# Kernel tuning notes

Measured on AMD Instinct MI355X. Metric: run time of the kernel, lower is better.

Reference implementation:

```python
import jax, jax.numpy as jnp
import numpy as np

HEAD_DIM = 128
NUM_BUCKETS = 32
MAX_DISTANCE = 128


def _rel_pos_bucket(seq_len):
    # T5 causal relative-position bucketing (lucidrains flash-pytorch version)
    pos = jnp.arange(seq_len)
    rel = pos[None, :] - pos[:, None]          # k_pos - q_pos
    n = jnp.maximum(-rel, 0)                   # causal: only past distances
    max_exact = NUM_BUCKETS // 2
    is_small = n < max_exact
    n_safe = jnp.maximum(n, 1).astype(jnp.float32)
    val_large = max_exact + (
        jnp.log(n_safe / max_exact) / np.log(MAX_DISTANCE / max_exact)
        * (NUM_BUCKETS - max_exact)
    ).astype(jnp.int32)
    val_large = jnp.minimum(val_large, NUM_BUCKETS - 1)
    return jnp.where(is_small, n, val_large)   # (S, S) int32


def setup_inputs() -> dict:
    key = jax.random.key(0)
    ks = jax.random.split(key, 10)
    B, S, D, I = 4, 2048, 768, 1536
    s = 0.02
    return {
        "x": jax.random.normal(ks[0], (B, S, D), jnp.float32),
        "v_W": jax.random.normal(ks[1], (D, I), jnp.float32) * s,
        "v_b": jnp.zeros((I,), jnp.float32),
        "g_W": jax.random.normal(ks[2], (D, I), jnp.float32) * s,
        "g_b": jnp.zeros((I,), jnp.float32),
        "in_W": jax.random.normal(ks[3], (D, HEAD_DIM), jnp.float32) * s,
        "in_b": jnp.zeros((HEAD_DIM,), jnp.float32),
        "q_gamma": jax.random.normal(ks[4], (HEAD_DIM,), jnp.float32) * s,
        "q_beta": jnp.zeros((HEAD_DIM,), jnp.float32),
        "k_gamma": jax.random.normal(ks[5], (HEAD_DIM,), jnp.float32) * s,
        "k_beta": jnp.zeros((HEAD_DIM,), jnp.float32),
        "out_W": jax.random.normal(ks[6], (I, D), jnp.float32) * s,
        "out_b": jnp.zeros((D,), jnp.float32),
        "rel_emb": jax.random.normal(ks[7], (NUM_BUCKETS, 1), jnp.float32) * s,
    }


def reference(x, v_W, v_b, g_W, g_b, in_W, in_b,
              q_gamma, q_beta, k_gamma, k_beta, out_W, out_b, rel_emb):
    silu = jax.nn.silu
    S = x.shape[1]
    v = silu(x @ v_W + v_b)                    # (B, S, I)
    gate = silu(x @ g_W + g_b)                 # (B, S, I)
    base = silu(x @ in_W + in_b)               # (B, S, 128)
    q = base * q_gamma + q_beta
    k = base * k_gamma + k_beta
    # scores scaled by sqrt(v dim) per torch code (v.size(-1) = inner_dim)
    attn = jnp.einsum('bns,bms->bnm', q, k) / jnp.sqrt(jnp.float32(v.shape[-1]))
    bias = rel_emb[_rel_pos_bucket(S), 0] * np.sqrt(HEAD_DIM)  # (S, S)
    attn = attn + bias
    causal = jnp.triu(jnp.ones((S, S), bool), 1)
    attn = jnp.where(causal, 0.0, attn)        # masked_fill to 0 before relu^2
    attn = jnp.square(jax.nn.relu(attn))       # ReLU^2 attention (no softmax)
    o = jnp.einsum('bnm,bme->bne', attn, v) * gate
    return o @ out_W + out_b                   # (B, S, D)
```

## Files before the change

### kernel.cpp

```cpp
#include <hip/hip_runtime.h>


typedef short short8 __attribute__((ext_vector_type(8)));
typedef float f32x4 __attribute__((ext_vector_type(4)));
typedef unsigned short us4 __attribute__((ext_vector_type(4)));
typedef float fl4 __attribute__((ext_vector_type(4)));

__device__ __forceinline__ unsigned short f2bf(float f) {
  unsigned u = __builtin_bit_cast(unsigned, f);
  u += 0x7FFFu + ((u >> 16) & 1u);
  return (unsigned short)(u >> 16);
}
__device__ __forceinline__ float bf2f(unsigned short b) {
  return __builtin_bit_cast(float, ((unsigned)b) << 16);
}
__device__ __forceinline__ float silu_f(float x) { return x / (1.0f + __expf(-x)); }

__device__ __forceinline__ void gl_lds16(const void* gp, void* lp) {
  __builtin_amdgcn_global_load_lds((const __attribute__((address_space(1))) void*)gp,
                                   (__attribute__((address_space(3))) void*)lp, 16, 0, 0);
}

template <int CALLS>
__device__ __forceinline__ void stage_sw(const unsigned short* __restrict__ g,
                                         int row_stride, int r0, int ko,
                                         unsigned short* lds, int w, int l) {
#pragma unroll
  for (int c = 0; c < CALLS; ++c) {
    int e = ((w * CALLS + c) << 9) + l * 8;
    int row = e >> 6;
    int gcol = ((((e >> 3) & 7) ^ (row & 7)) << 3);
    gl_lds16(g + (size_t)(r0 + row) * row_stride + (ko + gcol), lds + e);
  }
}
__device__ __forceinline__ void stage_sw128(const unsigned short* __restrict__ g, int r0,
                                            unsigned short* lds, int w, int l) {
#pragma unroll
  for (int c = 0; c < 8; ++c) {
    int e = ((w * 8 + c) << 9) + l * 8;
    int row = e >> 7;
    int gcol = ((((e >> 3) & 15) ^ (row & 7)) << 3);
    gl_lds16(g + (size_t)(r0 + row) * 128 + gcol, lds + e);
  }
}

__device__ __forceinline__ void mfma_sw(const unsigned short* As, const unsigned short* Bs,
                                        f32x4 acc[4][4], int wm, int wn, int quad, int lc) {
  const int x7 = lc & 7;
#pragma unroll
  for (int kk = 0; kk < 2; ++kk) {
    short8 af[4], bfr[4];
#pragma unroll
    for (int i = 0; i < 4; ++i)
      af[i] = *(const short8*)&As[(wm + i * 16 + lc) * 64 + (((kk * 4 + quad) ^ x7) << 3)];
#pragma unroll
    for (int j = 0; j < 4; ++j)
      bfr[j] = *(const short8*)&Bs[(wn + j * 16 + lc) * 64 + (((kk * 4 + quad) ^ x7) << 3)];
#pragma unroll
    for (int i = 0; i < 4; ++i)
#pragma unroll
      for (int j = 0; j < 4; ++j)
        acc[i][j] = __builtin_amdgcn_mfma_f32_16x16x32_bf16(af[i], bfr[j], acc[i][j], 0, 0, 0);
  }
}

__global__ __launch_bounds__(256, 2) void g123_k(
    const unsigned short* __restrict__ X,
    const unsigned short* __restrict__ Wst,
    unsigned short* __restrict__ vt,
    unsigned short* __restrict__ gateT,
    unsigned short* __restrict__ wq,
    unsigned short* __restrict__ wk,
    const float* __restrict__ v_b, const float* __restrict__ g_b,
    const float* __restrict__ in_b, const float* __restrict__ q_g,
    const float* __restrict__ q_be, const float* __restrict__ k_g,
    const float* __restrict__ k_be) {
  __shared__ unsigned short As[256 * 64];
  __shared__ unsigned short Bs[128 * 64];
  const int t = threadIdx.x, l = t & 63, w = t >> 6;
  const int id = blockIdx.x;
  const int xcd = id & 7, rest = id >> 3;
  const int n = rest % 25, m = (rest / 25) * 8 + xcd;
  const int m0 = m * 256, n0 = n * 128;
  const int wm = (w >> 1) * 128, wn = (w & 1) * 64;
  const int quad = l >> 4, lr = quad * 4, lc = l & 15;
  const int x7 = lc & 7;

  f32x4 acc[8][4] = {};
  for (int ko = 0; ko < 768; ko += 64) {
    stage_sw<8>(X, 768, m0, ko, As, w, l);
    stage_sw<4>(Wst, 768, n0, ko, Bs, w, l);
    __syncthreads();
#pragma unroll
    for (int kk = 0; kk < 2; ++kk) {
      short8 af[8], bfr[4];
#pragma unroll
      for (int i = 0; i < 8; ++i)
        af[i] = *(const short8*)&As[(wm + i * 16 + lc) * 64 + (((kk * 4 + quad) ^ x7) << 3)];
#pragma unroll
      for (int j = 0; j < 4; ++j)
        bfr[j] = *(const short8*)&Bs[(wn + j * 16 + lc) * 64 + (((kk * 4 + quad) ^ x7) << 3)];
#pragma unroll
      for (int i = 0; i < 8; ++i)
#pragma unroll
        for (int j = 0; j < 4; ++j)
          acc[i][j] = __builtin_amdgcn_mfma_f32_16x16x32_bf16(af[i], bfr[j], acc[i][j], 0, 0, 0);
    }
    __syncthreads();
  }

#pragma unroll
  for (int i = 0; i < 8; ++i) {
    const int gm = m0 + wm + i * 16 + lr;
#pragma unroll
    for (int j = 0; j < 4; ++j) {
      const int gn = n0 + wn + j * 16 + lc;
      f32x4 a = acc[i][j];
      if (n0 < 1536) {
        float bv = v_b[gn];
        us4 pk;
#pragma unroll
        for (int r = 0; r < 4; ++r) pk[r] = f2bf(silu_f(a[r] + bv));
        size_t off = (size_t)(gm >> 11) * (1536 * 2048) + (size_t)gn * 2048 + (gm & 2047);
        *(us4*)&vt[off] = pk;
      } else if (n0 < 3072) {
        float bv = g_b[gn - 1536];
        us4 pk;
#pragma unroll
        for (int r = 0; r < 4; ++r) pk[r] = f2bf(silu_f(a[r] + bv));
        *(us4*)&gateT[(size_t)(gn - 1536) * 8192 + gm] = pk;
      } else {
        int h = gn - 3072;
        float bb = in_b[h], qg = q_g[h], qb = q_be[h], kg = k_g[h], kb = k_be[h];
#pragma unroll
        for (int r = 0; r < 4; ++r) {
          float s = silu_f(a[r] + bb);
          wq[(size_t)(gm + r) * 128 + h] = f2bf(s * qg + qb);
          wk[(size_t)(gm + r) * 128 + h] = f2bf(s * kg + kb);
        }
      }
    }
  }
}

__global__ __launch_bounds__(256) void scores_k(
    const unsigned short* __restrict__ wk, const unsigned short* __restrict__ wq,
    unsigned short* __restrict__ P, const float* __restrict__ btab) {
  __shared__ unsigned short As[128 * 128];
  __shared__ unsigned short Bs[128 * 128];
  const int t = threadIdx.x, l = t & 63, w = t >> 6;
  const int z = blockIdx.z;
  int ti = blockIdx.x;
  int r = (int)((sqrtf((float)(8 * ti + 1)) - 1.0f) * 0.5f);
  if ((r + 1) * (r + 2) / 2 <= ti) ++r;
  int c = ti - r * (r + 1) / 2;
  const int m0 = c * 128, n0 = r * 128;
  const unsigned short* A = wk + (size_t)z * 2048 * 128;
  const unsigned short* Bt = wq + (size_t)z * 2048 * 128;
  unsigned short* Pz = P + (size_t)z * 2048 * 2048;
  const int wm = (w >> 1) * 64, wn = (w & 1) * 64;
  const int quad = l >> 4, lr = quad * 4, lc = l & 15;
  const int x7 = lc & 7;

  stage_sw128(A, m0, As, w, l);
  stage_sw128(Bt, n0, Bs, w, l);
  __syncthreads();

  f32x4 acc[4][4] = {};
#pragma unroll
  for (int kk = 0; kk < 4; ++kk) {
    short8 af[4], bfr[4];
#pragma unroll
    for (int i = 0; i < 4; ++i)
      af[i] = *(const short8*)&As[(wm + i * 16 + lc) * 128 + (((kk * 4 + quad) ^ x7) << 3)];
#pragma unroll
    for (int j = 0; j < 4; ++j)
      bfr[j] = *(const short8*)&Bs[(wn + j * 16 + lc) * 128 + (((kk * 4 + quad) ^ x7) << 3)];
#pragma unroll
    for (int i = 0; i < 4; ++i)
#pragma unroll
      for (int j = 0; j < 4; ++j)
        acc[i][j] = __builtin_amdgcn_mfma_f32_16x16x32_bf16(af[i], bfr[j], acc[i][j], 0, 0, 0);
  }

  const float SCALE = 0.025515518153991442f;
#pragma unroll
  for (int i = 0; i < 4; ++i) {
    const int gm = m0 + wm + i * 16 + lr;
#pragma unroll
    for (int j = 0; j < 4; ++j) {
      const int gn = n0 + wn + j * 16 + lc;
      us4 pk;
#pragma unroll
      for (int r2 = 0; r2 < 4; ++r2) {
        int mm = gm + r2;
        float v = 0.0f;
        if (mm <= gn) {
          float tt = fmaf(acc[i][j][r2], SCALE, btab[gn - mm]);
          tt = fmaxf(tt, 0.0f);
          v = tt * tt;
        }
        pk[r2] = f2bf(v);
      }
      *(us4*)&Pz[(size_t)gn * 2048 + gm] = pk;
    }
  }
}

__global__ __launch_bounds__(256) void og_k(
    const unsigned short* __restrict__ Vt,
    const unsigned short* __restrict__ P,
    const unsigned short* __restrict__ gateT,
    unsigned short* __restrict__ og) {
  __shared__ unsigned short As[128 * 64];
  __shared__ unsigned short Bs[128 * 64];
  const int t = threadIdx.x, l = t & 63, w = t >> 6;
  const int id = blockIdx.x;
  const int bblk = id / 96, rr = id % 96;
  const int xcd = rr & 7, mi = rr >> 3;
  const int half = xcd >> 2, z = xcd & 3;
  const int nt = 15 - 2 * bblk - (half ^ (bblk & 1));
  const int m0 = mi * 128;
  const int n0 = nt * 128;
  const int kend = n0 + 128;
  const unsigned short* A = Vt + (size_t)z * 1536 * 2048;
  const unsigned short* B = P + (size_t)z * 2048 * 2048;
  const int wm = (w >> 1) * 64, wn = (w & 1) * 64;
  const int quad = l >> 4, lr = quad * 4, lc = l & 15;

  f32x4 acc[4][4] = {};
  for (int ko = 0; ko < kend; ko += 64) {
    stage_sw<4>(A, 2048, m0, ko, As, w, l);
    stage_sw<4>(B, 2048, n0, ko, Bs, w, l);
    __syncthreads();
    mfma_sw(As, Bs, acc, wm, wn, quad, lc);
    __syncthreads();
  }
#pragma unroll
  for (int i = 0; i < 4; ++i) {
    const int gm = m0 + wm + i * 16 + lr;
#pragma unroll
    for (int j = 0; j < 4; ++j) {
      const int gn = n0 + wn + j * 16 + lc;
      us4 pk;
#pragma unroll
      for (int r2 = 0; r2 < 4; ++r2) {
        float g = bf2f(gateT[(size_t)(gm + r2) * 8192 + z * 2048 + gn]);
        pk[r2] = f2bf(acc[i][j][r2] * g);
      }
      *(us4*)&og[((size_t)z * 2048 + gn) * 1536 + gm] = pk;
    }
  }
}

__global__ __launch_bounds__(256) void gout_k(
    const unsigned short* __restrict__ A,
    const unsigned short* __restrict__ Bt,
    float* __restrict__ out, const float* __restrict__ o_b) {
  __shared__ unsigned short As[64 * 64];
  __shared__ unsigned short Bs[128 * 64];
  const int t = threadIdx.x, l = t & 63, w = t >> 6;
  const int id = blockIdx.x;
  const int xcd = id & 7, rest = id >> 3;
  const int m = rest % 12, ng = rest / 12;
  const int m0 = m * 64, n0 = (ng * 8 + xcd) * 128;
  const int wm = (w >> 1) * 32, wn = (w & 1) * 64;
  const int quad = l >> 4, lr = quad * 4, lc = l & 15;
  const int x7 = lc & 7;

  f32x4 acc[2][4] = {};
  for (int ko = 0; ko < 1536; ko += 64) {
    stage_sw<2>(A, 1536, m0, ko, As, w, l);
    stage_sw<4>(Bt, 1536, n0, ko, Bs, w, l);
    __syncthreads();
#pragma unroll
    for (int kk = 0; kk < 2; ++kk) {
      short8 af[2], bfr[4];
#pragma unroll
      for (int i = 0; i < 2; ++i)
        af[i] = *(const short8*)&As[(wm + i * 16 + lc) * 64 + (((kk * 4 + quad) ^ x7) << 3)];
#pragma unroll
      for (int j = 0; j < 4; ++j)
        bfr[j] = *(const short8*)&Bs[(wn + j * 16 + lc) * 64 + (((kk * 4 + quad) ^ x7) << 3)];
#pragma unroll
      for (int i = 0; i < 2; ++i)
#pragma unroll
        for (int j = 0; j < 4; ++j)
          acc[i][j] = __builtin_amdgcn_mfma_f32_16x16x32_bf16(af[i], bfr[j], acc[i][j], 0, 0, 0);
    }
    __syncthreads();
  }
#pragma unroll
  for (int i = 0; i < 2; ++i) {
    const int gm = m0 + wm + i * 16 + lr;
#pragma unroll
    for (int j = 0; j < 4; ++j) {
      const int gn = n0 + wn + j * 16 + lc;
      fl4 ob = *(const fl4*)&o_b[gm];
      fl4 res;
#pragma unroll
      for (int r2 = 0; r2 < 4; ++r2) res[r2] = acc[i][j][r2] + ob[r2];
      *(fl4*)&out[(size_t)gn * 768 + gm] = res;
    }
  }
}

__global__ void cvt_bf16(const float* __restrict__ in, unsigned short* __restrict__ out, int n) {
  int i = (blockIdx.x * blockDim.x + threadIdx.x) * 4;
  if (i < n) {
    fl4 v = *(const fl4*)&in[i];
    us4 o;
#pragma unroll
    for (int r = 0; r < 4; ++r) o[r] = f2bf(v[r]);
    *(us4*)&out[i] = o;
  }
}

__global__ void transpose_cvt4(const float* __restrict__ s0, unsigned short* __restrict__ d0,
                               const float* __restrict__ s1, unsigned short* __restrict__ d1,
                               const float* __restrict__ s2, unsigned short* __restrict__ d2,
                               const float* __restrict__ s3, unsigned short* __restrict__ d3,
                               const float* __restrict__ rel_emb, float* __restrict__ tab) {
  if (blockIdx.z == 4) {
    if (blockIdx.x == 0 && blockIdx.y == 0) {
      int d = threadIdx.y * 32 + threadIdx.x;
#pragma unroll
      for (int rep = 0; rep < 8; ++rep, d += 256) {
        int bucket;
        if (d < 16) {
          bucket = d;
        } else {
          float n = (float)d;
          int vl = 16 + (int)((logf(n * 0.0625f) / logf(8.0f)) * 16.0f);
          bucket = vl < 31 ? vl : 31;
        }
        tab[d] = rel_emb[bucket] * 11.3137085f;
      }
    }
    return;
  }
  __shared__ float tile[32][33];
  const float* in;
  unsigned short* out;
  int K_, N_, bxm, bym;
  switch (blockIdx.z) {
    case 0: in = s0; out = d0; K_ = 768; N_ = 1536; bxm = 48; bym = 24; break;
    case 1: in = s1; out = d1; K_ = 768; N_ = 1536; bxm = 48; bym = 24; break;
    case 2: in = s2; out = d2; K_ = 768; N_ = 128;  bxm = 4;  bym = 24; break;
    default: in = s3; out = d3; K_ = 1536; N_ = 768; bxm = 24; bym = 48; break;
  }
  if ((int)blockIdx.x >= bxm || (int)blockIdx.y >= bym) return;
  int bn = blockIdx.x * 32, bk = blockIdx.y * 32;
  int tx = threadIdx.x, ty = threadIdx.y;
#pragma unroll
  for (int i2 = 0; i2 < 32; i2 += 8)
    tile[ty + i2][tx] = in[(size_t)(bk + ty + i2) * N_ + (bn + tx)];
  __syncthreads();
#pragma unroll
  for (int i2 = 0; i2 < 32; i2 += 8)
    out[(size_t)(bn + ty + i2) * K_ + (bk + tx)] = f2bf(tile[tx][ty + i2]);
}

extern "C" void kernel_launch(void* const* d_in, const int* in_sizes, int n_in,
                              void* d_out, int out_size, void* d_ws, size_t ws_size,
                              hipStream_t stream) {
  const float* x    = (const float*)d_in[0];
  const float* vW   = (const float*)d_in[1];
  const float* v_b  = (const float*)d_in[2];
  const float* gW   = (const float*)d_in[3];
  const float* g_b  = (const float*)d_in[4];
  const float* inW  = (const float*)d_in[5];
  const float* in_b = (const float*)d_in[6];
  const float* q_g  = (const float*)d_in[7];
  const float* q_be = (const float*)d_in[8];
  const float* k_g  = (const float*)d_in[9];
  const float* k_be = (const float*)d_in[10];
  const float* oW   = (const float*)d_in[11];
  const float* o_b  = (const float*)d_in[12];
  const float* rel  = (const float*)d_in[13];

  char* p = (char*)d_ws;
  auto alloc = [&](size_t bytes) -> char* {
    char* r = p;
    p += (bytes + 255) & ~(size_t)255;
    return r;
  };
  unsigned short* x_bf   = (unsigned short*)alloc(8192ull * 768 * 2);
  unsigned short* wstack = (unsigned short*)alloc(3200ull * 768 * 2);
  unsigned short* vWt  = wstack;
  unsigned short* gWt  = wstack + 1536ull * 768;
  unsigned short* inWt = wstack + 3072ull * 768;
  unsigned short* oWt  = (unsigned short*)alloc(768ull * 1536 * 2);
  unsigned short* wq   = (unsigned short*)alloc(8192ull * 128 * 2);
  unsigned short* wk   = (unsigned short*)alloc(8192ull * 128 * 2);
  unsigned short* vt   = (unsigned short*)alloc(4ull * 1536 * 2048 * 2);
  unsigned short* gateT= (unsigned short*)alloc(1536ull * 8192 * 2);
  unsigned short* P    = (unsigned short*)alloc(4ull * 2048 * 2048 * 2);
  unsigned short* og   = (unsigned short*)alloc(8192ull * 1536 * 2);
  float* btab          = (float*)alloc(2048 * 4);

  cvt_bf16<<<dim3(6144), dim3(256), 0, stream>>>(x, x_bf, 8192 * 768);
  transpose_cvt4<<<dim3(48, 48, 5), dim3(32, 8), 0, stream>>>(vW, vWt, gW, gWt, inW, inWt,
                                                              oW, oWt, rel, btab);

  g123_k<<<dim3(800), 256, 0, stream>>>(x_bf, wstack, vt, gateT, wq, wk,
                                        v_b, g_b, in_b, q_g, q_be, k_g, k_be);
  scores_k<<<dim3(136, 1, 4), 256, 0, stream>>>(wk, wq, P, btab);
  og_k<<<dim3(768), 256, 0, stream>>>(vt, P, gateT, og);
  gout_k<<<dim3(768), 256, 0, stream>>>(oWt, og, (float*)d_out, o_b);
}
```

Before: 288.6 us.

## Replace LDS-staged GEMM tiles with direct global-to-register fragment loads

The three main GEMM kernels (projection, attention-times-V, output) drop the shared-memory staging and barriers. Each lane now loads its MFMA operand fragments straight from global memory, with one-step register double buffering. The projection kernel's M tile is halved to 128 and the grid doubled to keep the same coverage. This removes LDS traffic and synchronisation, but gives up cross-wave data reuse. Each operand is now fetched several times from global memory or L2, and the 16-byte per-lane loads have poor coalescing.

```diff
diff --git a/kernel.cpp b/kernel.cpp
--- a/kernel.cpp
+++ b/kernel.cpp
@@ -20,19 +20,8 @@
   __builtin_amdgcn_global_load_lds((const __attribute__((address_space(1))) void*)gp,
                                    (__attribute__((address_space(3))) void*)lp, 16, 0, 0);
 }
-
-template <int CALLS>
-__device__ __forceinline__ void stage_sw(const unsigned short* __restrict__ g,
-                                         int row_stride, int r0, int ko,
-                                         unsigned short* lds, int w, int l) {
-#pragma unroll
-  for (int c = 0; c < CALLS; ++c) {
-    int e = ((w * CALLS + c) << 9) + l * 8;
-    int row = e >> 6;
-    int gcol = ((((e >> 3) & 7) ^ (row & 7)) << 3);
-    gl_lds16(g + (size_t)(r0 + row) * row_stride + (ko + gcol), lds + e);
-  }
-}
+__device__ __forceinline__ short8 s8(fl4 v) { return __builtin_bit_cast(short8, v); }
+
 __device__ __forceinline__ void stage_sw128(const unsigned short* __restrict__ g, int r0,
                                             unsigned short* lds, int w, int l) {
 #pragma unroll
@@ -44,27 +33,7 @@
   }
 }
 
-__device__ __forceinline__ void mfma_sw(const unsigned short* As, const unsigned short* Bs,
-                                        f32x4 acc[4][4], int wm, int wn, int quad, int lc) {
-  const int x7 = lc & 7;
-#pragma unroll
-  for (int kk = 0; kk < 2; ++kk) {
-    short8 af[4], bfr[4];
-#pragma unroll
-    for (int i = 0; i < 4; ++i)
-      af[i] = *(const short8*)&As[(wm + i * 16 + lc) * 64 + (((kk * 4 + quad) ^ x7) << 3)];
-#pragma unroll
-    for (int j = 0; j < 4; ++j)
-      bfr[j] = *(const short8*)&Bs[(wn + j * 16 + lc) * 64 + (((kk * 4 + quad) ^ x7) << 3)];
-#pragma unroll
-    for (int i = 0; i < 4; ++i)
-#pragma unroll
-      for (int j = 0; j < 4; ++j)
-        acc[i][j] = __builtin_amdgcn_mfma_f32_16x16x32_bf16(af[i], bfr[j], acc[i][j], 0, 0, 0);
-  }
-}
-
-__global__ __launch_bounds__(256, 2) void g123_k(
+__global__ __launch_bounds__(256) void g123_k(
     const unsigned short* __restrict__ X,
     const unsigned short* __restrict__ Wst,
     unsigned short* __restrict__ vt,
@@ -75,42 +44,42 @@
     const float* __restrict__ in_b, const float* __restrict__ q_g,
     const float* __restrict__ q_be, const float* __restrict__ k_g,
     const float* __restrict__ k_be) {
-  __shared__ unsigned short As[256 * 64];
-  __shared__ unsigned short Bs[128 * 64];
   const int t = threadIdx.x, l = t & 63, w = t >> 6;
   const int id = blockIdx.x;
   const int xcd = id & 7, rest = id >> 3;
   const int n = rest % 25, m = (rest / 25) * 8 + xcd;
-  const int m0 = m * 256, n0 = n * 128;
-  const int wm = (w >> 1) * 128, wn = (w & 1) * 64;
+  const int m0 = m * 128, n0 = n * 128;
+  const int wm = (w >> 1) * 64, wn = (w & 1) * 64;
   const int quad = l >> 4, lr = quad * 4, lc = l & 15;
-  const int x7 = lc & 7;
-
-  f32x4 acc[8][4] = {};
-  for (int ko = 0; ko < 768; ko += 64) {
-    stage_sw<8>(X, 768, m0, ko, As, w, l);
-    stage_sw<4>(Wst, 768, n0, ko, Bs, w, l);
-    __syncthreads();
-#pragma unroll
-    for (int kk = 0; kk < 2; ++kk) {
-      short8 af[8], bfr[4];
-#pragma unroll
-      for (int i = 0; i < 8; ++i)
-        af[i] = *(const short8*)&As[(wm + i * 16 + lc) * 64 + (((kk * 4 + quad) ^ x7) << 3)];
+
+  const unsigned short* ap[4];
+  const unsigned short* bp[4];
+#pragma unroll
+  for (int i = 0; i < 4; ++i) ap[i] = X + (size_t)(m0 + wm + i * 16 + lc) * 768 + quad * 8;
+#pragma unroll
+  for (int j = 0; j < 4; ++j) bp[j] = Wst + (size_t)(n0 + wn + j * 16 + lc) * 768 + quad * 8;
+
+  fl4 ca[4], cb[4], na[4], nb[4];
+#pragma unroll
+  for (int i = 0; i < 4; ++i) { ca[i] = *(const fl4*)ap[i]; cb[i] = *(const fl4*)bp[i]; }
+  f32x4 acc[4][4] = {};
+  for (int ks = 0; ks < 24; ++ks) {
+    if (ks < 23) {
+      const int off = (ks + 1) * 32;
+#pragma unroll
+      for (int i = 0; i < 4; ++i) { na[i] = *(const fl4*)(ap[i] + off); nb[i] = *(const fl4*)(bp[i] + off); }
+    }
+#pragma unroll
+    for (int i = 0; i < 4; ++i)
 #pragma unroll
       for (int j = 0; j < 4; ++j)
-        bfr[j] = *(const short8*)&Bs[(wn + j * 16 + lc) * 64 + (((kk * 4 + quad) ^ x7) << 3)];
-#pragma unroll
-      for (int i = 0; i < 8; ++i)
-#pragma unroll
-        for (int j = 0; j < 4; ++j)
-          acc[i][j] = __builtin_amdgcn_mfma_f32_16x16x32_bf16(af[i], bfr[j], acc[i][j], 0, 0, 0);
-    }
-    __syncthreads();
-  }
-
-#pragma unroll
-  for (int i = 0; i < 8; ++i) {
+        acc[i][j] = __builtin_amdgcn_mfma_f32_16x16x32_bf16(s8(ca[i]), s8(cb[j]), acc[i][j], 0, 0, 0);
+#pragma unroll
+    for (int i = 0; i < 4; ++i) { ca[i] = na[i]; cb[i] = nb[i]; }
+  }
+
+#pragma unroll
+  for (int i = 0; i < 4; ++i) {
     const int gm = m0 + wm + i * 16 + lr;
 #pragma unroll
     for (int j = 0; j < 4; ++j) {
@@ -212,8 +181,6 @@
     const unsigned short* __restrict__ P,
     const unsigned short* __restrict__ gateT,
     unsigned short* __restrict__ og) {
-  __shared__ unsigned short As[128 * 64];
-  __shared__ unsigned short Bs[128 * 64];
   const int t = threadIdx.x, l = t & 63, w = t >> 6;
   const int id = blockIdx.x;
   const int bblk = id / 96, rr = id % 96;
@@ -222,19 +189,36 @@
   const int nt = 15 - 2 * bblk - (half ^ (bblk & 1));
   const int m0 = mi * 128;
   const int n0 = nt * 128;
-  const int kend = n0 + 128;
+  const int T = (n0 + 128) >> 5;
   const unsigned short* A = Vt + (size_t)z * 1536 * 2048;
   const unsigned short* B = P + (size_t)z * 2048 * 2048;
   const int wm = (w >> 1) * 64, wn = (w & 1) * 64;
   const int quad = l >> 4, lr = quad * 4, lc = l & 15;
 
+  const unsigned short* ap[4];
+  const unsigned short* bp[4];
+#pragma unroll
+  for (int i = 0; i < 4; ++i) ap[i] = A + (size_t)(m0 + wm + i * 16 + lc) * 2048 + quad * 8;
+#pragma unroll
+  for (int j = 0; j < 4; ++j) bp[j] = B + (size_t)(n0 + wn + j * 16 + lc) * 2048 + quad * 8;
+
+  fl4 ca[4], cb[4], na[4], nb[4];
+#pragma unroll
+  for (int i = 0; i < 4; ++i) { ca[i] = *(const fl4*)ap[i]; cb[i] = *(const fl4*)bp[i]; }
   f32x4 acc[4][4] = {};
-  for (int ko = 0; ko < kend; ko += 64) {
-    stage_sw<4>(A, 2048, m0, ko, As, w, l);
-    stage_sw<4>(B, 2048, n0, ko, Bs, w, l);
-    __syncthreads();
-    mfma_sw(As, Bs, acc, wm, wn, quad, lc);
-    __syncthreads();
+  for (int ks = 0; ks < T; ++ks) {
+    if (ks + 1 < T) {
+      const int off = (ks + 1) * 32;
+#pragma unroll
+      for (int i = 0; i < 4; ++i) { na[i] = *(const fl4*)(ap[i] + off); nb[i] = *(const fl4*)(bp[i] + off); }
+    }
+#pragma unroll
+    for (int i = 0; i < 4; ++i)
+#pragma unroll
+      for (int j = 0; j < 4; ++j)
+        acc[i][j] = __builtin_amdgcn_mfma_f32_16x16x32_bf16(s8(ca[i]), s8(cb[j]), acc[i][j], 0, 0, 0);
+#pragma unroll
+    for (int i = 0; i < 4; ++i) { ca[i] = na[i]; cb[i] = nb[i]; }
   }
 #pragma unroll
   for (int i = 0; i < 4; ++i) {
@@ -257,8 +241,6 @@
     const unsigned short* __restrict__ A,
     const unsigned short* __restrict__ Bt,
     float* __restrict__ out, const float* __restrict__ o_b) {
-  __shared__ unsigned short As[64 * 64];
-  __shared__ unsigned short Bs[128 * 64];
   const int t = threadIdx.x, l = t & 63, w = t >> 6;
   const int id = blockIdx.x;
   const int xcd = id & 7, rest = id >> 3;
@@ -266,29 +248,37 @@
   const int m0 = m * 64, n0 = (ng * 8 + xcd) * 128;
   const int wm = (w >> 1) * 32, wn = (w & 1) * 64;
   const int quad = l >> 4, lr = quad * 4, lc = l & 15;
-  const int x7 = lc & 7;
-
+
+  const unsigned short* ap[2];
+  const unsigned short* bp[4];
+#pragma unroll
+  for (int i = 0; i < 2; ++i) ap[i] = A + (size_t)(m0 + wm + i * 16 + lc) * 1536 + quad * 8;
+#pragma unroll
+  for (int j = 0; j < 4; ++j) bp[j] = Bt + (size_t)(n0 + wn + j * 16 + lc) * 1536 + quad * 8;
+
+  fl4 ca[2], cb[4], na[2], nb[4];
+#pragma unroll
+  for (int i = 0; i < 2; ++i) ca[i] = *(const fl4*)ap[i];
+#pragma unroll
+  for (int j = 0; j < 4; ++j) cb[j] = *(const fl4*)bp[j];
   f32x4 acc[2][4] = {};
-  for (int ko = 0; ko < 1536; ko += 64) {
-    stage_sw<2>(A, 1536, m0, ko, As, w, l);
-    stage_sw<4>(Bt, 1536, n0, ko, Bs, w, l);
-    __syncthreads();
-#pragma unroll
-    for (int kk = 0; kk < 2; ++kk) {
-      short8 af[2], bfr[4];
-#pragma unroll
-      for (int i = 0; i < 2; ++i)
-        af[i] = *(const short8*)&As[(wm + i * 16 + lc) * 64 + (((kk * 4 + quad) ^ x7) << 3)];
+  for (int ks = 0; ks < 48; ++ks) {
+    if (ks < 47) {
+      const int off = (ks + 1) * 32;
+#pragma unroll
+      for (int i = 0; i < 2; ++i) na[i] = *(const fl4*)(ap[i] + off);
+#pragma unroll
+      for (int j = 0; j < 4; ++j) nb[j] = *(const fl4*)(bp[j] + off);
+    }
+#pragma unroll
+    for (int i = 0; i < 2; ++i)
 #pragma unroll
       for (int j = 0; j < 4; ++j)
-        bfr[j] = *(const short8*)&Bs[(wn + j * 16 + lc) * 64 + (((kk * 4 + quad) ^ x7) << 3)];
-#pragma unroll
-      for (int i = 0; i < 2; ++i)
-#pragma unroll
-        for (int j = 0; j < 4; ++j)
-          acc[i][j] = __builtin_amdgcn_mfma_f32_16x16x32_bf16(af[i], bfr[j], acc[i][j], 0, 0, 0);
-    }
-    __syncthreads();
+        acc[i][j] = __builtin_amdgcn_mfma_f32_16x16x32_bf16(s8(ca[i]), s8(cb[j]), acc[i][j], 0, 0, 0);
+#pragma unroll
+    for (int i = 0; i < 2; ++i) ca[i] = na[i];
+#pragma unroll
+    for (int j = 0; j < 4; ++j) cb[j] = nb[j];
   }
 #pragma unroll
   for (int i = 0; i < 2; ++i) {
@@ -403,8 +393,8 @@
   transpose_cvt4<<<dim3(48, 48, 5), dim3(32, 8), 0, stream>>>(vW, vWt, gW, gWt, inW, inWt,
                                                               oW, oWt, rel, btab);
 
-  g123_k<<<dim3(800), 256, 0, stream>>>(x_bf, wstack, vt, gateT, wq, wk,
-                                        v_b, g_b, in_b, q_g, q_be, k_g, k_be);
+  g123_k<<<dim3(1600), 256, 0, stream>>>(x_bf, wstack, vt, gateT, wq, wk,
+                                         v_b, g_b, in_b, q_g, q_be, k_g, k_be);
   scores_k<<<dim3(136, 1, 4), 256, 0, stream>>>(wk, wq, P, btab);
   og_k<<<dim3(768), 256, 0, stream>>>(vt, P, gateT, og);
   gout_k<<<dim3(768), 256, 0, stream>>>(oWt, og, (float*)d_out, o_b);
```

Result: slower. 525.5 us (+82.1%).
